# Optimization experiments

Measured on AMD Instinct MI355X. Metric: run time of the kernel, lower is better.

## Reference

```python
import jax, jax.numpy as jnp
import numpy as np

B, S, D, H = 4, 2048, 1024, 16
DK = D // H

def setup_inputs() -> dict:
    key = jax.random.key(0)
    ks = jax.random.split(key, 11)
    s = 1.0 / np.sqrt(D)
    return {
        "query": jax.random.normal(ks[0], (B, S, D), jnp.float32),
        "key_": jax.random.normal(ks[1], (B, S, D), jnp.float32),
        "value": jax.random.normal(ks[2], (B, S, D), jnp.float32),
        "Wq": jax.random.uniform(ks[3], (D, D), jnp.float32, -s, s),
        "bq": jax.random.uniform(ks[4], (D,), jnp.float32, -s, s),
        "Wk": jax.random.uniform(ks[5], (D, D), jnp.float32, -s, s),
        "bk": jax.random.uniform(ks[6], (D,), jnp.float32, -s, s),
        "Wv": jax.random.uniform(ks[7], (D, D), jnp.float32, -s, s),
        "bv": jax.random.uniform(ks[8], (D,), jnp.float32, -s, s),
        "Wo": jax.random.uniform(ks[9], (D, D), jnp.float32, -s, s),
        "bo": jax.random.uniform(ks[10], (D,), jnp.float32, -s, s),
    }

def _split_heads(x):
    # [B,S,D] -> [B,H,S,DK]
    b, s, _ = x.shape
    return x.reshape(b, s, H, DK).transpose(0, 2, 1, 3)

def reference(query, key_, value, Wq, bq, Wk, bk, Wv, bv, Wo, bo):
    Q = _split_heads(query @ Wq.T + bq)
    K = _split_heads(key_ @ Wk.T + bk)
    V = _split_heads(value @ Wv.T + bv)
    scores = jnp.einsum('bhqd,bhkd->bhqk', Q, K) / np.sqrt(DK).astype(np.float32)
    attn = jax.nn.softmax(scores, axis=-1)
    ctx = jnp.einsum('bhqk,bhkd->bhqd', attn, V)  # [B,H,S,DK]
    ctx = ctx.transpose(0, 2, 1, 3).reshape(query.shape[0], -1, D)
    return ctx @ Wo.T + bo
```

## Files before the change

kernel.cpp:

```cpp
#include <hip/hip_runtime.h>
#include <hip/hip_bf16.h>
#include <math.h>


#define B_SZ   4
#define S_LEN  2048
#define D_DIM  1024
#define NH     16
#define DKD    64
#define M_TOT  (B_SZ * S_LEN)

typedef __bf16 bf16_t;
typedef bf16_t bf16x8 __attribute__((ext_vector_type(8)));
typedef bf16_t bf16x4 __attribute__((ext_vector_type(4)));
typedef float  f32x4  __attribute__((ext_vector_type(4)));

typedef __attribute__((address_space(1))) void gvoid;
typedef __attribute__((address_space(3))) void lvoid;

extern "C" __device__ float __ocml_native_exp2_f32(float);

__global__ __launch_bounds__(256)
void cvt_kernel(const float* __restrict__ src, bf16_t* __restrict__ dst, int n4)
{
    const int i = blockIdx.x * blockDim.x + threadIdx.x;
    if (i < n4) {
        f32x4 v = *(const f32x4*)(src + (size_t)i * 4);
        bf16x4 o;
        #pragma unroll
        for (int j = 0; j < 4; ++j) o[j] = (bf16_t)v[j];
        *(bf16x4*)(dst + (size_t)i * 4) = o;
    }
}

template <typename OutT, bool TR, int BN>
__global__ __launch_bounds__(256, 4)
void gemm_bt_bias(const bf16_t* __restrict__ A, const bf16_t* __restrict__ Bt,
                  const float* __restrict__ bias, OutT* __restrict__ C, float ascale)
{
    constexpr int K = 1024, N = 1024;
    constexpr int BM = 128, BK = 32;
    constexpr int NJ = BN / 32;

    __shared__ __align__(16) bf16_t lA[BM * BK];
    __shared__ __align__(16) bf16_t lB[BN * BK];

    const int tid  = threadIdx.x;
    const int wave = tid >> 6;
    const int lane = tid & 63;

    const int row0 = blockIdx.x * BM;
    const int col0 = blockIdx.y * BN;

    const int wr = (wave >> 1) * 64;
    const int wc = (wave & 1) * (BN / 2);

    f32x4 acc[4][NJ] = {};

    const int frow = lane & 15;
    const int kq   = (lane >> 4) * 8;

    for (int k0 = 0; k0 < K; k0 += BK) {
        __syncthreads();
        #pragma unroll
        for (int c = 0; c < 2; ++c) {
            const int chunk = c * 4 + wave;
            const int e     = chunk * 512 + lane * 8;
            const int r     = e >> 5;
            const int kk    = e & 31;
            __builtin_amdgcn_global_load_lds((gvoid*)(A + (size_t)(row0 + r) * K + k0 + kk),
                                             (lvoid*)(lA + chunk * 512), 16, 0, 0);
        }
        #pragma unroll
        for (int cb = 0; cb < BN / 64; ++cb) {
            const int chunk = cb * 4 + wave;
            const int e     = chunk * 512 + lane * 8;
            const int r     = e >> 5;
            const int kk    = e & 31;
            __builtin_amdgcn_global_load_lds((gvoid*)(Bt + (size_t)(col0 + r) * K + k0 + kk),
                                             (lvoid*)(lB + chunk * 512), 16, 0, 0);
        }
        __syncthreads();

        bf16x8 af[4], bfr[NJ];
        #pragma unroll
        for (int i = 0; i < 4; ++i)
            af[i] = *(const bf16x8*)(lA + (wr + i * 16 + frow) * BK + kq);
        #pragma unroll
        for (int j = 0; j < NJ; ++j)
            bfr[j] = *(const bf16x8*)(lB + (wc + j * 16 + frow) * BK + kq);
        #pragma unroll
        for (int i = 0; i < 4; ++i)
            #pragma unroll
            for (int j = 0; j < NJ; ++j)
                acc[i][j] = __builtin_amdgcn_mfma_f32_16x16x32_bf16(af[i], bfr[j], acc[i][j], 0, 0, 0);
    }

    const int rb   = (lane >> 4) * 4;
    const int ccol = lane & 15;
    #pragma unroll
    for (int j = 0; j < NJ; ++j) {
        const int n = col0 + wc + j * 16 + ccol;
        const float bv = bias[n];
        #pragma unroll
        for (int i = 0; i < 4; ++i) {
            const int m = row0 + wr + i * 16 + rb;
            if constexpr (TR) {
                bf16x4 o4;
                #pragma unroll
                for (int r = 0; r < 4; ++r) o4[r] = (bf16_t)((acc[i][j][r] + bv) * ascale);
                *(bf16x4*)((bf16_t*)C + (size_t)n * M_TOT + m) = o4;
            } else {
                #pragma unroll
                for (int r = 0; r < 4; ++r)
                    C[(size_t)(m + r) * N + n] = (OutT)((acc[i][j][r] + bv) * ascale);
            }
        }
    }
}

__global__ __launch_bounds__(256, 4)
void attn_mfma(const bf16_t* __restrict__ Qg, const bf16_t* __restrict__ Kg,
               const bf16_t* __restrict__ Vt, bf16_t* __restrict__ ctx)
{
    constexpr int PSTR = 72;
    __shared__ __align__(16) bf16_t lK[64 * PSTR];
    __shared__ __align__(16) bf16_t lV[64 * PSTR];
    __shared__ __align__(16) bf16_t lP[4][32 * PSTR];

    const int tid  = threadIdx.x;
    const int wave = tid >> 6;
    const int lane = tid & 63;
    const int qd   = lane >> 4;
    const int c    = lane & 15;

    const int bh   = blockIdx.x >> 4;
    const int qblk = blockIdx.x & 15;
    const int b    = bh >> 4;
    const int h    = bh & 15;

    const int q0 = qblk * 128 + wave * 32;

    const bf16_t* Qb = Qg + ((size_t)(b * S_LEN + q0)) * D_DIM + h * DKD;
    const bf16_t* Kb = Kg + ((size_t)(b * S_LEN)) * D_DIM + h * DKD;
    const bf16_t* Vb = Vt + ((size_t)(h * DKD)) * M_TOT + b * S_LEN;

    bf16_t* Pw = &lP[wave][0];

    bf16x8 qf[2][2];
    #pragma unroll
    for (int qt = 0; qt < 2; ++qt)
        #pragma unroll
        for (int ks = 0; ks < 2; ++ks)
            qf[qt][ks] = *(const bf16x8*)(Qb + (size_t)(qt * 16 + c) * D_DIM + ks * 32 + qd * 8);

    bf16x8 ones;
    #pragma unroll
    for (int i = 0; i < 8; ++i) ones[i] = (bf16_t)1.0f;

    f32x4 oacc[4][2] = {};
    f32x4 lacc[2]    = {};

    for (int kt = 0; kt < S_LEN; kt += 64) {
        __syncthreads();
        #pragma unroll
        for (int cc = 0; cc < 2; ++cc) {
            const int ch  = cc * 256 + tid;
            const int row = ch >> 3;
            const int c8  = ch & 7;
            bf16x8 kv = *(const bf16x8*)(Kb + (size_t)(kt + row) * D_DIM + c8 * 8);
            bf16x8 vv = *(const bf16x8*)(Vb + (size_t)row * M_TOT + kt + c8 * 8);
            *(bf16x8*)(lK + row * PSTR + c8 * 8) = kv;
            *(bf16x8*)(lV + row * PSTR + c8 * 8) = vv;
        }
        __syncthreads();

        bf16x8 kf[4][2];
        #pragma unroll
        for (int i = 0; i < 4; ++i)
            #pragma unroll
            for (int ks = 0; ks < 2; ++ks)
                kf[i][ks] = *(const bf16x8*)(lK + (i * 16 + c) * PSTR + ks * 32 + qd * 8);

        f32x4 st[4][2] = {};
        #pragma unroll
        for (int ks = 0; ks < 2; ++ks)
            #pragma unroll
            for (int i = 0; i < 4; ++i)
                #pragma unroll
                for (int qt = 0; qt < 2; ++qt)
                    st[i][qt] = __builtin_amdgcn_mfma_f32_16x16x32_bf16(kf[i][ks], qf[qt][ks], st[i][qt], 0, 0, 0);

        bf16x8 vf[4][2];
        #pragma unroll
        for (int fm = 0; fm < 4; ++fm)
            #pragma unroll
            for (int ks = 0; ks < 2; ++ks)
                vf[fm][ks] = *(const bf16x8*)(lV + (fm * 16 + c) * PSTR + ks * 32 + qd * 8);

        #pragma unroll
        for (int i = 0; i < 4; ++i)
            #pragma unroll
            for (int qt = 0; qt < 2; ++qt) {
                bf16x4 pw;
                #pragma unroll
                for (int r = 0; r < 4; ++r)
                    pw[r] = (bf16_t)__ocml_native_exp2_f32(st[i][qt][r]);
                *(bf16x4*)(Pw + (qt * 16 + c) * PSTR + i * 16 + qd * 4) = pw;
            }

        #pragma unroll
        for (int qn = 0; qn < 2; ++qn)
            #pragma unroll
            for (int ks = 0; ks < 2; ++ks) {
                bf16x8 pf = *(const bf16x8*)(Pw + (qn * 16 + c) * PSTR + ks * 32 + qd * 8);
                lacc[qn] = __builtin_amdgcn_mfma_f32_16x16x32_bf16(ones, pf, lacc[qn], 0, 0, 0);
                #pragma unroll
                for (int fm = 0; fm < 4; ++fm)
                    oacc[fm][qn] = __builtin_amdgcn_mfma_f32_16x16x32_bf16(vf[fm][ks], pf, oacc[fm][qn], 0, 0, 0);
            }
    }

    #pragma unroll
    for (int qn = 0; qn < 2; ++qn) {
        const float linv = 1.0f / lacc[qn][0];
        bf16_t* op = ctx + ((size_t)(b * S_LEN + q0 + qn * 16 + c)) * D_DIM + h * DKD + qd * 4;
        #pragma unroll
        for (int fm = 0; fm < 4; ++fm) {
            bf16x4 o4;
            #pragma unroll
            for (int r = 0; r < 4; ++r) o4[r] = (bf16_t)(oacc[fm][qn][r] * linv);
            *(bf16x4*)(op + fm * 16) = o4;
        }
    }
}

extern "C" void kernel_launch(void* const* d_in, const int* in_sizes, int n_in,
                              void* d_out, int out_size, void* d_ws, size_t ws_size,
                              hipStream_t stream)
{
    const float* query = (const float*)d_in[0];
    const float* key_  = (const float*)d_in[1];
    const float* value = (const float*)d_in[2];
    const float* Wq    = (const float*)d_in[3];
    const float* bq    = (const float*)d_in[4];
    const float* Wk    = (const float*)d_in[5];
    const float* bk    = (const float*)d_in[6];
    const float* Wv    = (const float*)d_in[7];
    const float* bv    = (const float*)d_in[8];
    const float* Wo    = (const float*)d_in[9];
    const float* bo    = (const float*)d_in[10];
    float* out = (float*)d_out;

    const size_t mat  = (size_t)M_TOT * D_DIM;
    const size_t wmat = (size_t)D_DIM * D_DIM;

    bf16_t* t0 = (bf16_t*)d_ws;
    bf16_t* w0 = t0 + mat;
    bf16_t* Qw = w0 + wmat;
    bf16_t* Kw = Qw + mat;
    bf16_t* Vt = Kw + mat;

    const int gcvt_m = (int)(mat  / 4 / 256);
    const int gcvt_w = (int)(wmat / 4 / 256);
    dim3 gg(M_TOT / 128, D_DIM / 64);

    const float qscale = 0.18033688011112042f;

    cvt_kernel<<<gcvt_m, 256, 0, stream>>>(query, t0, (int)(mat / 4));
    cvt_kernel<<<gcvt_w, 256, 0, stream>>>(Wq, w0, (int)(wmat / 4));
    gemm_bt_bias<bf16_t, false, 64><<<gg, 256, 0, stream>>>(t0, w0, bq, Qw, qscale);

    cvt_kernel<<<gcvt_m, 256, 0, stream>>>(key_, t0, (int)(mat / 4));
    cvt_kernel<<<gcvt_w, 256, 0, stream>>>(Wk, w0, (int)(wmat / 4));
    gemm_bt_bias<bf16_t, false, 64><<<gg, 256, 0, stream>>>(t0, w0, bk, Kw, 1.0f);

    cvt_kernel<<<gcvt_m, 256, 0, stream>>>(value, t0, (int)(mat / 4));
    cvt_kernel<<<gcvt_w, 256, 0, stream>>>(Wv, w0, (int)(wmat / 4));
    gemm_bt_bias<bf16_t, true, 64><<<gg, 256, 0, stream>>>(t0, w0, bv, Vt, 1.0f);

    attn_mfma<<<dim3(B_SZ * NH * (S_LEN / 128)), 256, 0, stream>>>(Qw, Kw, Vt, t0);

    cvt_kernel<<<gcvt_w, 256, 0, stream>>>(Wo, w0, (int)(wmat / 4));
    gemm_bt_bias<float, false, 64><<<gg, 256, 0, stream>>>(t0, w0, bo, out, 1.0f);
}
```

Before: 366.6 us.

## Fuse fp32-to-bf16 activation conversion into a batched QKV GEMM with larger tiles

Removes the separate activation conversion kernels by loading fp32 activations directly in the GEMM, converting them in registers and storing bf16 to LDS, with a register prefetch of the next K tile. The three Q/K/V projections are merged into one launch over a z grid dimension, and the output tile grows from 128x64 to 128x128 for both GEMMs. This cuts an fp32 read plus bf16 write and re-read of each activation matrix, along with several launches. In exchange it doubles fp32 A traffic per tile and raises register pressure, with launch bounds relaxed to allow fewer blocks per SM.

```diff
diff --git a/kernel.cpp b/kernel.cpp
--- a/kernel.cpp
+++ b/kernel.cpp
@@ -33,17 +33,27 @@
     }
 }
 
-template <typename OutT, bool TR, int BN>
-__global__ __launch_bounds__(256, 4)
-void gemm_bt_bias(const bf16_t* __restrict__ A, const bf16_t* __restrict__ Bt,
-                  const float* __restrict__ bias, OutT* __restrict__ C, float ascale)
+__global__ __launch_bounds__(256, 2)
+void qkv_gemm(const float* __restrict__ Aq, const float* __restrict__ Ak,
+              const float* __restrict__ Av,
+              const bf16_t* __restrict__ Wqb, const bf16_t* __restrict__ Wkb,
+              const bf16_t* __restrict__ Wvb,
+              const float* __restrict__ bq, const float* __restrict__ bk,
+              const float* __restrict__ bv,
+              bf16_t* __restrict__ Qw, bf16_t* __restrict__ Kw,
+              bf16_t* __restrict__ Vt, float qscale)
 {
     constexpr int K = 1024, N = 1024;
-    constexpr int BM = 128, BK = 32;
-    constexpr int NJ = BN / 32;
+    constexpr int BM = 128, BN = 128, BK = 32;
 
     __shared__ __align__(16) bf16_t lA[BM * BK];
     __shared__ __align__(16) bf16_t lB[BN * BK];
+
+    const int z = blockIdx.z;
+    const float* A  = (z == 0) ? Aq : (z == 1) ? Ak : Av;
+    const bf16_t* W = (z == 0) ? Wqb : (z == 1) ? Wkb : Wvb;
+    const float* bias = (z == 0) ? bq : (z == 1) ? bk : bv;
+    const float scale = (z == 0) ? qscale : 1.0f;
 
     const int tid  = threadIdx.x;
     const int wave = tid >> 6;
@@ -53,9 +63,114 @@
     const int col0 = blockIdx.y * BN;
 
     const int wr = (wave >> 1) * 64;
-    const int wc = (wave & 1) * (BN / 2);
-
-    f32x4 acc[4][NJ] = {};
+    const int wc = (wave & 1) * 64;
+
+    f32x4 acc[4][4] = {};
+
+    const int frow = lane & 15;
+    const int kq   = (lane >> 4) * 8;
+
+    const int r0c = tid >> 2;
+    const int k0c = (tid & 3) * 8;
+    const int r1c = (256 + tid) >> 2;
+    const int k1c = k0c;
+
+    f32x4 pa[2][2];
+    {
+        const float* g0 = A + (size_t)(row0 + r0c) * K + k0c;
+        const float* g1 = A + (size_t)(row0 + r1c) * K + k1c;
+        pa[0][0] = *(const f32x4*)g0;  pa[0][1] = *(const f32x4*)(g0 + 4);
+        pa[1][0] = *(const f32x4*)g1;  pa[1][1] = *(const f32x4*)(g1 + 4);
+    }
+
+    for (int k0 = 0; k0 < K; k0 += BK) {
+        __syncthreads();
+        #pragma unroll
+        for (int p = 0; p < 2; ++p) {
+            bf16x8 a8;
+            #pragma unroll
+            for (int j = 0; j < 4; ++j) {
+                a8[j]     = (bf16_t)pa[p][0][j];
+                a8[4 + j] = (bf16_t)pa[p][1][j];
+            }
+            *(bf16x8*)(lA + (p * 256 + tid) * 8) = a8;
+        }
+        #pragma unroll
+        for (int c = 0; c < 2; ++c) {
+            const int chunk = c * 4 + wave;
+            const int e     = chunk * 512 + lane * 8;
+            const int rr    = e >> 5;
+            const int kk    = e & 31;
+            __builtin_amdgcn_global_load_lds((gvoid*)(W + (size_t)(col0 + rr) * K + k0 + kk),
+                                             (lvoid*)(lB + chunk * 512), 16, 0, 0);
+        }
+        __syncthreads();
+
+        if (k0 + BK < K) {
+            const float* g0 = A + (size_t)(row0 + r0c) * K + (k0 + BK) + k0c;
+            const float* g1 = A + (size_t)(row0 + r1c) * K + (k0 + BK) + k1c;
+            pa[0][0] = *(const f32x4*)g0;  pa[0][1] = *(const f32x4*)(g0 + 4);
+            pa[1][0] = *(const f32x4*)g1;  pa[1][1] = *(const f32x4*)(g1 + 4);
+        }
+
+        bf16x8 af[4], bfr[4];
+        #pragma unroll
+        for (int i = 0; i < 4; ++i) {
+            af[i]  = *(const bf16x8*)(lA + (wr + i * 16 + frow) * BK + kq);
+            bfr[i] = *(const bf16x8*)(lB + (wc + i * 16 + frow) * BK + kq);
+        }
+        #pragma unroll
+        for (int i = 0; i < 4; ++i)
+            #pragma unroll
+            for (int j = 0; j < 4; ++j)
+                acc[i][j] = __builtin_amdgcn_mfma_f32_16x16x32_bf16(af[i], bfr[j], acc[i][j], 0, 0, 0);
+    }
+
+    const int rb   = (lane >> 4) * 4;
+    const int ccol = lane & 15;
+    #pragma unroll
+    for (int j = 0; j < 4; ++j) {
+        const int n = col0 + wc + j * 16 + ccol;
+        const float bvv = bias[n];
+        #pragma unroll
+        for (int i = 0; i < 4; ++i) {
+            const int m = row0 + wr + i * 16 + rb;
+            if (z == 2) {
+                bf16x4 o4;
+                #pragma unroll
+                for (int r = 0; r < 4; ++r) o4[r] = (bf16_t)(acc[i][j][r] + bvv);
+                *(bf16x4*)(Vt + (size_t)n * M_TOT + m) = o4;
+            } else {
+                bf16_t* Cp = (z == 0) ? Qw : Kw;
+                #pragma unroll
+                for (int r = 0; r < 4; ++r)
+                    Cp[(size_t)(m + r) * N + n] = (bf16_t)((acc[i][j][r] + bvv) * scale);
+            }
+        }
+    }
+}
+
+__global__ __launch_bounds__(256, 2)
+void gemm_out(const bf16_t* __restrict__ A, const bf16_t* __restrict__ Bt,
+              const float* __restrict__ bias, float* __restrict__ C)
+{
+    constexpr int K = 1024, N = 1024;
+    constexpr int BM = 128, BK = 32;
+
+    __shared__ __align__(16) bf16_t lA[BM * BK];
+    __shared__ __align__(16) bf16_t lB[128 * BK];
+
+    const int tid  = threadIdx.x;
+    const int wave = tid >> 6;
+    const int lane = tid & 63;
+
+    const int row0 = blockIdx.x * BM;
+    const int col0 = blockIdx.y * 128;
+
+    const int wr = (wave >> 1) * 64;
+    const int wc = (wave & 1) * 64;
+
+    f32x4 acc[4][4] = {};
 
     const int frow = lane & 15;
     const int kq   = (lane >> 4) * 8;
@@ -70,51 +185,36 @@
             const int kk    = e & 31;
             __builtin_amdgcn_global_load_lds((gvoid*)(A + (size_t)(row0 + r) * K + k0 + kk),
                                              (lvoid*)(lA + chunk * 512), 16, 0, 0);
-        }
-        #pragma unroll
-        for (int cb = 0; cb < BN / 64; ++cb) {
-            const int chunk = cb * 4 + wave;
-            const int e     = chunk * 512 + lane * 8;
-            const int r     = e >> 5;
-            const int kk    = e & 31;
             __builtin_amdgcn_global_load_lds((gvoid*)(Bt + (size_t)(col0 + r) * K + k0 + kk),
                                              (lvoid*)(lB + chunk * 512), 16, 0, 0);
         }
         __syncthreads();
 
-        bf16x8 af[4], bfr[NJ];
+        bf16x8 af[4], bfr[4];
+        #pragma unroll
+        for (int i = 0; i < 4; ++i) {
+            af[i]  = *(const bf16x8*)(lA + (wr + i * 16 + frow) * BK + kq);
+            bfr[i] = *(const bf16x8*)(lB + (wc + i * 16 + frow) * BK + kq);
+        }
         #pragma unroll
         for (int i = 0; i < 4; ++i)
-            af[i] = *(const bf16x8*)(lA + (wr + i * 16 + frow) * BK + kq);
-        #pragma unroll
-        for (int j = 0; j < NJ; ++j)
-            bfr[j] = *(const bf16x8*)(lB + (wc + j * 16 + frow) * BK + kq);
-        #pragma unroll
-        for (int i = 0; i < 4; ++i)
-            #pragma unroll
-            for (int j = 0; j < NJ; ++j)
+            #pragma unroll
+            for (int j = 0; j < 4; ++j)
                 acc[i][j] = __builtin_amdgcn_mfma_f32_16x16x32_bf16(af[i], bfr[j], acc[i][j], 0, 0, 0);
     }
 
     const int rb   = (lane >> 4) * 4;
     const int ccol = lane & 15;
     #pragma unroll
-    for (int j = 0; j < NJ; ++j) {
+    for (int j = 0; j < 4; ++j) {
         const int n = col0 + wc + j * 16 + ccol;
-        const float bv = bias[n];
+        const float bvv = bias[n];
         #pragma unroll
         for (int i = 0; i < 4; ++i) {
             const int m = row0 + wr + i * 16 + rb;
-            if constexpr (TR) {
-                bf16x4 o4;
-                #pragma unroll
-                for (int r = 0; r < 4; ++r) o4[r] = (bf16_t)((acc[i][j][r] + bv) * ascale);
-                *(bf16x4*)((bf16_t*)C + (size_t)n * M_TOT + m) = o4;
-            } else {
-                #pragma unroll
-                for (int r = 0; r < 4; ++r)
-                    C[(size_t)(m + r) * N + n] = (OutT)((acc[i][j][r] + bv) * ascale);
-            }
+            #pragma unroll
+            for (int r = 0; r < 4; ++r)
+                C[(size_t)(m + r) * N + n] = acc[i][j][r] + bvv;
         }
     }
 }
@@ -260,27 +360,21 @@
     bf16_t* Qw = w0 + wmat;
     bf16_t* Kw = Qw + mat;
     bf16_t* Vt = Kw + mat;
-
-    const int gcvt_m = (int)(mat  / 4 / 256);
+    bf16_t* w1 = t0;
+    bf16_t* w2 = t0 + wmat;
+
     const int gcvt_w = (int)(wmat / 4 / 256);
-    dim3 gg(M_TOT / 128, D_DIM / 64);
-
     const float qscale = 0.18033688011112042f;
 
-    cvt_kernel<<<gcvt_m, 256, 0, stream>>>(query, t0, (int)(mat / 4));
     cvt_kernel<<<gcvt_w, 256, 0, stream>>>(Wq, w0, (int)(wmat / 4));
-    gemm_bt_bias<bf16_t, false, 64><<<gg, 256, 0, stream>>>(t0, w0, bq, Qw, qscale);
-
-    cvt_kernel<<<gcvt_m, 256, 0, stream>>>(key_, t0, (int)(mat / 4));
-    cvt_kernel<<<gcvt_w, 256, 0, stream>>>(Wk, w0, (int)(wmat / 4));
-    gemm_bt_bias<bf16_t, false, 64><<<gg, 256, 0, stream>>>(t0, w0, bk, Kw, 1.0f);
-
-    cvt_kernel<<<gcvt_m, 256, 0, stream>>>(value, t0, (int)(mat / 4));
-    cvt_kernel<<<gcvt_w, 256, 0, stream>>>(Wv, w0, (int)(wmat / 4));
-    gemm_bt_bias<bf16_t, true, 64><<<gg, 256, 0, stream>>>(t0, w0, bv, Vt, 1.0f);
+    cvt_kernel<<<gcvt_w, 256, 0, stream>>>(Wk, w1, (int)(wmat / 4));
+    cvt_kernel<<<gcvt_w, 256, 0, stream>>>(Wv, w2, (int)(wmat / 4));
+
+    qkv_gemm<<<dim3(M_TOT / 128, D_DIM / 128, 3), 256, 0, stream>>>(
+        query, key_, value, w0, w1, w2, bq, bk, bv, Qw, Kw, Vt, qscale);
 
     attn_mfma<<<dim3(B_SZ * NH * (S_LEN / 128)), 256, 0, stream>>>(Qw, Kw, Vt, t0);
 
     cvt_kernel<<<gcvt_w, 256, 0, stream>>>(Wo, w0, (int)(wmat / 4));
-    gemm_bt_bias<float, false, 64><<<gg, 256, 0, stream>>>(t0, w0, bo, out, 1.0f);
-}
+    gemm_out<<<dim3(M_TOT / 128, D_DIM / 128), 256, 0, stream>>>(t0, w0, bo, out);
+}
```

Result: faster. 356.1 us (-2.9%).
